# Performance work log

Measured on AMD Instinct MI355X. Metric: run time of the kernel, lower is better.

The kernel has to match this reference:

```python
import jax, jax.numpy as jnp
import numpy as np

D_MODEL = 1024
NUM_HEADS = 16
D_K = D_MODEL // NUM_HEADS  # 64
THETA = 10000.0


def apply_rope(x, positions, theta):
    # x: [b, h, s, d_k]; interleaved-pair RoPE
    d = x.shape[-1]
    inv_freq = theta ** (-jnp.arange(0, d, 2, dtype=jnp.float32) / d)  # [d/2]
    angles = positions.astype(jnp.float32)[:, None] * inv_freq[None, :]  # [s, d/2]
    cos = jnp.cos(angles)
    sin = jnp.sin(angles)
    x1 = x[..., 0::2]
    x2 = x[..., 1::2]
    out_even = x1 * cos - x2 * sin
    out_odd = x1 * sin + x2 * cos
    return jnp.stack([out_even, out_odd], axis=-1).reshape(x.shape)


def setup_inputs() -> dict:
    key = jax.random.key(0)
    kx, kq, kk, kv, ko = jax.random.split(key, 5)
    scale = 1.0 / np.sqrt(D_MODEL)
    return {
        "x": jax.random.normal(kx, (1, 4096, D_MODEL), dtype=jnp.float32),
        "Wq": jax.random.normal(kq, (D_MODEL, D_MODEL), dtype=jnp.float32) * scale,
        "Wk": jax.random.normal(kk, (D_MODEL, D_MODEL), dtype=jnp.float32) * scale,
        "Wv": jax.random.normal(kv, (D_MODEL, D_MODEL), dtype=jnp.float32) * scale,
        "Wo": jax.random.normal(ko, (D_MODEL, D_MODEL), dtype=jnp.float32) * scale,
    }


def reference(x, Wq, Wk, Wv, Wo):
    b, s, _ = x.shape
    # Linear (no bias, weight stored as [out, in]): y = x @ W^T
    q = jnp.einsum("bsd,ed->bse", x, Wq).reshape(b, s, NUM_HEADS, D_K).transpose(0, 2, 1, 3)
    k = jnp.einsum("bsd,ed->bse", x, Wk).reshape(b, s, NUM_HEADS, D_K).transpose(0, 2, 1, 3)
    v = jnp.einsum("bsd,ed->bse", x, Wv).reshape(b, s, NUM_HEADS, D_K).transpose(0, 2, 1, 3)

    positions = jnp.arange(s)
    q = apply_rope(q, positions, THETA)
    k = apply_rope(k, positions, THETA)

    scores = jnp.einsum("bhqd,bhkd->bhqk", q, k) / jnp.sqrt(jnp.float32(D_K))
    causal = jnp.tril(jnp.ones((s, s), dtype=bool))
    scores = jnp.where(causal, scores, -jnp.inf)
    probs = jax.nn.softmax(scores, axis=-1)
    ctx = jnp.einsum("bhqk,bhkd->bhqd", probs, v)  # [b,h,s,d_k]
    ctx = ctx.transpose(0, 2, 1, 3).reshape(b, s, D_MODEL)
    return jnp.einsum("bse,de->bsd", ctx, Wo)
```

## Files before the change

kernel.cpp:

```cpp
#include <hip/hip_runtime.h>
#include <hip/hip_bf16.h>
#include <math.h>


#define S_LEN 4096
#define DMODEL 1024
#define NHEAD 16
#define QSCALE 0.1803368801111244f
#define PSTR 76

typedef __attribute__((ext_vector_type(8))) short short8;
typedef __attribute__((ext_vector_type(4))) short short4_t;
typedef __attribute__((ext_vector_type(2))) unsigned int uint2_t;
typedef __attribute__((ext_vector_type(4))) float floatx4;

static __device__ __forceinline__ void load_lds16(const void* g, void* l) {
    __builtin_amdgcn_global_load_lds((const __attribute__((address_space(1))) void*)g,
                                     (__attribute__((address_space(3))) void*)l, 16, 0, 0);
}

static __device__ __forceinline__ __hip_bfloat16 bf16_fast(float f) {
    unsigned int u = __builtin_bit_cast(unsigned int, f) + 0x8000u;
    unsigned short s = (unsigned short)(u >> 16);
    return __builtin_bit_cast(__hip_bfloat16, s);
}
static __device__ __forceinline__ unsigned int pack_bf16x2(float a, float b) {
    unsigned int ua = __builtin_bit_cast(unsigned int, a) + 0x8000u;
    unsigned int ub = __builtin_bit_cast(unsigned int, b) + 0x8000u;
    return __builtin_amdgcn_perm(ub, ua, 0x07060302);
}

__global__ void cvt_all_kernel(const float* __restrict__ x,  const float* __restrict__ wq,
                               const float* __restrict__ wk, const float* __restrict__ wv,
                               const float* __restrict__ wo,
                               __hip_bfloat16* __restrict__ xb,  __hip_bfloat16* __restrict__ wqb,
                               __hip_bfloat16* __restrict__ wkb, __hip_bfloat16* __restrict__ wvb,
                               __hip_bfloat16* __restrict__ wob)
{
    const size_t NX = (size_t)S_LEN * DMODEL;
    const size_t NW = (size_t)DMODEL * DMODEL;
    size_t t = ((size_t)blockIdx.x * blockDim.x + threadIdx.x) * 4;
    const float* src; __hip_bfloat16* dst; size_t off;
    if (t < NX) { src = x; dst = xb; off = t; }
    else {
        size_t j = t - NX; int seg = (int)(j >> 20); off = j & (NW - 1);
        src = (seg == 0) ? wq : (seg == 1) ? wk : (seg == 2) ? wv : wo;
        dst = (seg == 0) ? wqb : (seg == 1) ? wkb : (seg == 2) ? wvb : wob;
    }
    float4 v = *(const float4*)(src + off);
    uint2_t w;
    w.x = pack_bf16x2(v.x, v.y);
    w.y = pack_bf16x2(v.z, v.w);
    *(uint2_t*)(dst + off) = w;
}

__global__ __launch_bounds__(256) void qkv_gemm(
    const __hip_bfloat16* __restrict__ A,
    const __hip_bfloat16* __restrict__ Bq,
    const __hip_bfloat16* __restrict__ Bk,
    const __hip_bfloat16* __restrict__ Bv,
    __hip_bfloat16* __restrict__ Qb,
    __hip_bfloat16* __restrict__ Kb,
    __hip_bfloat16* __restrict__ Vtb)
{
    __shared__ __hip_bfloat16 As[128 * 32];
    __shared__ __hip_bfloat16 Bs[128 * 32];
    const int tid  = threadIdx.x;
    const int wave = tid >> 6;
    const int lane = tid & 63;
    const int quad = lane >> 4;
    const int l15  = lane & 15;
    const int sec  = blockIdx.x >> 3;
    const __hip_bfloat16* B = (sec == 0) ? Bq : (sec == 1) ? Bk : Bv;
    const int n0 = (blockIdx.x & 7) * 128;
    const int m0 = blockIdx.y * 128;
    const int wm = (wave & 1) * 64;
    const int wn = (wave >> 1) * 64;

    floatx4 acc[4][4] = {};

    for (int kt = 0; kt < DMODEL; kt += 32) {
        #pragma unroll
        for (int p = 0; p < 2; ++p) {
            int base = (p * 4 + wave) * 1024;
            int b    = base + lane * 16;
            int row  = b >> 6;
            int ke   = (b & 63) >> 1;
            load_lds16(A + (size_t)(m0 + row) * DMODEL + kt + ke, (char*)As + base);
            load_lds16(B + (size_t)(n0 + row) * DMODEL + kt + ke, (char*)Bs + base);
        }
        __syncthreads();
        short8 af[4], bf[4];
        #pragma unroll
        for (int i = 0; i < 4; ++i)
            af[i] = *(const short8*)(As + (wm + i * 16 + l15) * 32 + quad * 8);
        #pragma unroll
        for (int j = 0; j < 4; ++j)
            bf[j] = *(const short8*)(Bs + (wn + j * 16 + l15) * 32 + quad * 8);
        #pragma unroll
        for (int i = 0; i < 4; ++i)
            #pragma unroll
            for (int j = 0; j < 4; ++j)
                acc[i][j] = __builtin_amdgcn_mfma_f32_16x16x32_bf16(af[i], bf[j], acc[i][j], 0, 0, 0);
        __syncthreads();
    }

    float ifreq[4];
    #pragma unroll
    for (int j = 0; j < 4; ++j) {
        int d = (j * 16 + l15) & 63;
        ifreq[j] = expf(-(float)(d & ~1) * (9.210340371976184f / 64.0f));
    }
    const float scale = (sec == 0) ? QSCALE : 1.0f;
    __hip_bfloat16* dst = (sec == 0) ? Qb : Kb;
    #pragma unroll
    for (int i = 0; i < 4; ++i) {
        int rowb = m0 + wm + i * 16 + quad * 4;
        #pragma unroll
        for (int j = 0; j < 4; ++j) {
            int col = n0 + wn + j * 16 + l15;
            int h   = col >> 6;
            int hd  = col & 63;
            if (sec == 2) {
                uint2_t w;
                w.x = pack_bf16x2(acc[i][j][0], acc[i][j][1]);
                w.y = pack_bf16x2(acc[i][j][2], acc[i][j][3]);
                int od = hd >> 4, lv = hd & 15;
                *(uint2_t*)(Vtb + (size_t)h * 262144 +
                            (((od * 512 + (rowb >> 3)) * 16 + lv) << 3) + (rowb & 7)) = w;
            } else {
                int g = hd >> 3, jj = hd & 7;
                #pragma unroll
                for (int r = 0; r < 4; ++r) {
                    int rr  = rowb + r;
                    float v = acc[i][j][r];
                    float ang = (float)rr * ifreq[j];
                    float sn, cs;
                    __sincosf(ang, &sn, &cs);
                    float pv  = __shfl_xor(v, 1);
                    float out = ((lane & 1) ? (pv * sn + v * cs)
                                            : (v * cs - pv * sn)) * scale;
                    dst[(size_t)h * 262144 +
                        ((((rr >> 4) * 8 + g) * 16 + (rr & 15)) << 3) + jj] = bf16_fast(out);
                }
            }
        }
    }
}

template<bool EDGE>
static __device__ __forceinline__ void attn_tile(
    int kt, int quad, int l15,
    const __hip_bfloat16* __restrict__ Kh, const __hip_bfloat16* __restrict__ Vh,
    const short8 aq[4][2], floatx4 o[4][4], float lp[4],
    __hip_bfloat16* __restrict__ PsW)
{
    asm volatile("s_waitcnt lgkmcnt(0)" ::: "memory");

    short8 kf[4][2], vf[4][2];
    #pragma unroll
    for (int ni = 0; ni < 4; ++ni)
        #pragma unroll
        for (int dc = 0; dc < 2; ++dc)
            kf[ni][dc] = *(const short8*)(Kh + (size_t)(((((kt*4 + ni)*8 + dc*4 + quad)*16 + l15) << 3)));
    #pragma unroll
    for (int od = 0; od < 4; ++od)
        #pragma unroll
        for (int dc = 0; dc < 2; ++dc)
            vf[od][dc] = *(const short8*)(Vh + (size_t)((((od*512 + kt*8 + dc*4 + quad)*16 + l15) << 3)));

    #pragma unroll
    for (int g = 0; g < 4; ++g) {
        __hip_bfloat16* strip = PsW + (g * 16 + l15) * PSTR;
        floatx4 st[4];
        #pragma unroll
        for (int ni = 0; ni < 4; ++ni) {
            floatx4 z = {};
            floatx4 s = __builtin_amdgcn_mfma_f32_16x16x32_bf16(kf[ni][0], aq[g][0], z, 0, 0, 0);
            st[ni]    = __builtin_amdgcn_mfma_f32_16x16x32_bf16(kf[ni][1], aq[g][1], s, 0, 0, 0);
        }
        #pragma unroll
        for (int ni = 0; ni < 4; ++ni) {
            float e[4];
            #pragma unroll
            for (int r = 0; r < 4; ++r) {
                float v = __builtin_amdgcn_exp2f(st[ni][r]);
                if (EDGE) {
                    if (ni * 16 + quad * 4 + r > g * 16 + l15) v = 0.0f;
                }
                e[r] = v;
            }
            lp[g] += (e[0] + e[1]) + (e[2] + e[3]);
            uint2_t w;
            w.x = pack_bf16x2(e[0], e[1]);
            w.y = pack_bf16x2(e[2], e[3]);
            *(short4_t*)(strip + ni * 16 + quad * 4) = __builtin_bit_cast(short4_t, w);
        }
        short8 ap[2];
        #pragma unroll
        for (int dc = 0; dc < 2; ++dc) {
            const __hip_bfloat16* pp = strip + dc * 32 + quad * 8;
            short4_t p0 = *(const short4_t*)pp;
            short4_t p1 = *(const short4_t*)(pp + 4);
            short8 a;
            a[0] = p0[0]; a[1] = p0[1]; a[2] = p0[2]; a[3] = p0[3];
            a[4] = p1[0]; a[5] = p1[1]; a[6] = p1[2]; a[7] = p1[3];
            ap[dc] = a;
        }
        #pragma unroll
        for (int od = 0; od < 4; ++od) {
            o[g][od] = __builtin_amdgcn_mfma_f32_16x16x32_bf16(ap[0], vf[od][0], o[g][od], 0, 0, 0);
            o[g][od] = __builtin_amdgcn_mfma_f32_16x16x32_bf16(ap[1], vf[od][1], o[g][od], 0, 0, 0);
        }
    }
}

__global__ __launch_bounds__(256, 2) void attn_kernel(
    const __hip_bfloat16* __restrict__ Q,
    const __hip_bfloat16* __restrict__ Kp,
    const __hip_bfloat16* __restrict__ Vp,
    __hip_bfloat16* __restrict__ CTX)
{
    __shared__ __hip_bfloat16 Buf[4][64 * PSTR];
    __shared__ float LPw[4][64];
    const int b  = blockIdx.x;
    const int h  = b & 15;
    const int u  = 63 - (b >> 4);
    const int tid  = threadIdx.x;
    const int wave = tid >> 6, lane = tid & 63;
    const int quad = lane >> 4, l15 = lane & 15;

    const __hip_bfloat16* Qh = Q  + (size_t)h * 262144;
    const __hip_bfloat16* Kh = Kp + (size_t)h * 262144;
    const __hip_bfloat16* Vh = Vp + (size_t)h * 262144;
    __hip_bfloat16* PsW = &Buf[wave][0];

    short8 aq[4][2];
    #pragma unroll
    for (int g = 0; g < 4; ++g)
        #pragma unroll
        for (int dc = 0; dc < 2; ++dc)
            aq[g][dc] = *(const short8*)(Qh + (size_t)(((((u*4 + g)*8 + dc*4 + quad)*16 + l15) << 3)));

    floatx4 o[4][4] = {};
    float lp[4] = {};

    for (int kt = wave; kt < u; kt += 4)
        attn_tile<false>(kt, quad, l15, Kh, Vh, aq, o, lp, PsW);
    if ((u & 3) == wave)
        attn_tile<true>(u, quad, l15, Kh, Vh, aq, o, lp, PsW);

    #pragma unroll
    for (int g = 0; g < 4; ++g) {
        float v = lp[g];
        v += __shfl_xor(v, 16);
        v += __shfl_xor(v, 32);
        lp[g] = v;
    }
    asm volatile("s_waitcnt lgkmcnt(0)" ::: "memory");
    if (quad == 0) {
        #pragma unroll
        for (int g = 0; g < 4; ++g)
            LPw[wave][g * 16 + l15] = lp[g];
    }
    #pragma unroll
    for (int g = 0; g < 4; ++g)
        #pragma unroll
        for (int od = 0; od < 4; ++od)
            #pragma unroll
            for (int r = 0; r < 4; ++r)
                Buf[wave][(g * 16 + quad * 4 + r) * PSTR + od * 16 + l15] =
                    bf16_fast(o[g][od][r]);
    __syncthreads();

    #pragma unroll
    for (int r = 0; r < 4; ++r) {
        int q = wave * 16 + quad * 4 + r;
        float ls = LPw[0][q] + LPw[1][q] + LPw[2][q] + LPw[3][q];
        float rl = __frcp_rn(ls);
        #pragma unroll
        for (int od = 0; od < 4; ++od) {
            float s = 0.0f;
            #pragma unroll
            for (int sl = 0; sl < 4; ++sl)
                s += __bfloat162float(Buf[sl][q * PSTR + od * 16 + l15]);
            CTX[(size_t)(u * 64 + q) * DMODEL + h * 64 + od * 16 + l15] =
                bf16_fast(s * rl);
        }
    }
}

__global__ __launch_bounds__(256) void out_gemm(
    const __hip_bfloat16* __restrict__ A,
    const __hip_bfloat16* __restrict__ B,
    float* __restrict__ C)
{
    __shared__ __hip_bfloat16 As[128 * 32];
    __shared__ __hip_bfloat16 Bs[64 * 32];
    const int tid  = threadIdx.x;
    const int wave = tid >> 6;
    const int lane = tid & 63;
    const int quad = lane >> 4;
    const int l15  = lane & 15;
    const int n0 = blockIdx.x * 64;
    const int m0 = blockIdx.y * 128;
    const int wm = (wave & 1) * 64;
    const int wn = (wave >> 1) * 32;

    floatx4 acc[4][2] = {};

    for (int kt = 0; kt < DMODEL; kt += 32) {
        #pragma unroll
        for (int p = 0; p < 3; ++p) {
            int id  = p * 4 + wave;
            if (id < 8) {
                int base = id * 1024;
                int b    = base + lane * 16;
                int row  = b >> 6;
                int ke   = (b & 63) >> 1;
                load_lds16(A + (size_t)(m0 + row) * DMODEL + kt + ke, (char*)As + base);
            } else {
                int base = (id - 8) * 1024;
                int b    = base + lane * 16;
                int row  = b >> 6;
                int ke   = (b & 63) >> 1;
                load_lds16(B + (size_t)(n0 + row) * DMODEL + kt + ke, (char*)Bs + base);
            }
        }
        __syncthreads();
        short8 af[4], bf[2];
        #pragma unroll
        for (int i = 0; i < 4; ++i)
            af[i] = *(const short8*)(As + (wm + i * 16 + l15) * 32 + quad * 8);
        #pragma unroll
        for (int j = 0; j < 2; ++j)
            bf[j] = *(const short8*)(Bs + (wn + j * 16 + l15) * 32 + quad * 8);
        #pragma unroll
        for (int i = 0; i < 4; ++i)
            #pragma unroll
            for (int j = 0; j < 2; ++j)
                acc[i][j] = __builtin_amdgcn_mfma_f32_16x16x32_bf16(af[i], bf[j], acc[i][j], 0, 0, 0);
        __syncthreads();
    }

    #pragma unroll
    for (int i = 0; i < 4; ++i) {
        int rowb = m0 + wm + i * 16 + quad * 4;
        #pragma unroll
        for (int j = 0; j < 2; ++j) {
            int col = n0 + wn + j * 16 + l15;
            #pragma unroll
            for (int r = 0; r < 4; ++r)
                C[(size_t)(rowb + r) * DMODEL + col] = acc[i][j][r];
        }
    }
}

extern "C" void kernel_launch(void* const* d_in, const int* in_sizes, int n_in,
                              void* d_out, int out_size, void* d_ws, size_t ws_size,
                              hipStream_t stream)
{
    const float* x  = (const float*)d_in[0];
    const float* Wq = (const float*)d_in[1];
    const float* Wk = (const float*)d_in[2];
    const float* Wv = (const float*)d_in[3];
    const float* Wo = (const float*)d_in[4];

    char* ws = (char*)d_ws;
    const size_t MB = 1024 * 1024;
    __hip_bfloat16* xb  = (__hip_bfloat16*)(ws);
    __hip_bfloat16* wqb = (__hip_bfloat16*)(ws +  8 * MB);
    __hip_bfloat16* wkb = (__hip_bfloat16*)(ws + 10 * MB);
    __hip_bfloat16* wvb = (__hip_bfloat16*)(ws + 12 * MB);
    __hip_bfloat16* wob = (__hip_bfloat16*)(ws + 14 * MB);
    __hip_bfloat16* Qb  = (__hip_bfloat16*)(ws + 16 * MB);
    __hip_bfloat16* Kbf = (__hip_bfloat16*)(ws + 24 * MB);
    __hip_bfloat16* Vtb = (__hip_bfloat16*)(ws + 32 * MB);
    __hip_bfloat16* Cx  = (__hip_bfloat16*)(ws + 40 * MB);

    cvt_all_kernel<<<8192, 256, 0, stream>>>(x, Wq, Wk, Wv, Wo, xb, wqb, wkb, wvb, wob);

    qkv_gemm<<<dim3(24, 32), 256, 0, stream>>>(xb, wqb, wkb, wvb, Qb, Kbf, Vtb);

    attn_kernel<<<1024, 256, 0, stream>>>(Qb, Kbf, Vtb, Cx);

    out_gemm<<<dim3(16, 32), 256, 0, stream>>>(Cx, wob, (float*)d_out);
}
```

Measured before the change: 202.4 us.

## Pre-swizzle bf16 operands in global memory and widen GEMM K-tile to 64

The conversion kernel and the attention epilogue now write the bf16 activations and weights with an XOR swizzle of 8-element groups inside each 64-wide K chunk. The GEMMs can then copy 64-wide K tiles straight into LDS with global_load_lds and read them without bank conflicts. Both QKV and output GEMMs double the K step to 64, halving the number of barrier pairs per tile at the cost of twice the LDS footprint. The conversion kernel also handles 8 elements per thread with half the blocks.

```diff
diff --git a/kernel.cpp b/kernel.cpp
--- a/kernel.cpp
+++ b/kernel.cpp
@@ -12,6 +12,7 @@
 typedef __attribute__((ext_vector_type(8))) short short8;
 typedef __attribute__((ext_vector_type(4))) short short4_t;
 typedef __attribute__((ext_vector_type(2))) unsigned int uint2_t;
+typedef __attribute__((ext_vector_type(4))) unsigned int uint4_t;
 typedef __attribute__((ext_vector_type(4))) float floatx4;
 
 static __device__ __forceinline__ void load_lds16(const void* g, void* l) {
@@ -39,7 +40,7 @@
 {
     const size_t NX = (size_t)S_LEN * DMODEL;
     const size_t NW = (size_t)DMODEL * DMODEL;
-    size_t t = ((size_t)blockIdx.x * blockDim.x + threadIdx.x) * 4;
+    size_t t = ((size_t)blockIdx.x * blockDim.x + threadIdx.x) * 8;
     const float* src; __hip_bfloat16* dst; size_t off;
     if (t < NX) { src = x; dst = xb; off = t; }
     else {
@@ -47,11 +48,18 @@
         src = (seg == 0) ? wq : (seg == 1) ? wk : (seg == 2) ? wv : wo;
         dst = (seg == 0) ? wqb : (seg == 1) ? wkb : (seg == 2) ? wvb : wob;
     }
-    float4 v = *(const float4*)(src + off);
-    uint2_t w;
-    w.x = pack_bf16x2(v.x, v.y);
-    w.y = pack_bf16x2(v.z, v.w);
-    *(uint2_t*)(dst + off) = w;
+    int row = (int)(off >> 10);
+    int k   = (int)(off & 1023);
+    int gp  = (((k >> 3) ^ row) & 7);
+    size_t doff = (off & ~(size_t)1023) + (size_t)((k & ~63) + (gp << 3));
+    float4 v0 = *(const float4*)(src + off);
+    float4 v1 = *(const float4*)(src + off + 4);
+    uint4_t w;
+    w.x = pack_bf16x2(v0.x, v0.y);
+    w.y = pack_bf16x2(v0.z, v0.w);
+    w.z = pack_bf16x2(v1.x, v1.y);
+    w.w = pack_bf16x2(v1.z, v1.w);
+    *(uint4_t*)(dst + doff) = w;
 }
 
 __global__ __launch_bounds__(256) void qkv_gemm(
@@ -63,13 +71,14 @@
     __hip_bfloat16* __restrict__ Kb,
     __hip_bfloat16* __restrict__ Vtb)
 {
-    __shared__ __hip_bfloat16 As[128 * 32];
-    __shared__ __hip_bfloat16 Bs[128 * 32];
+    __shared__ __hip_bfloat16 As[128 * 64];
+    __shared__ __hip_bfloat16 Bs[128 * 64];
     const int tid  = threadIdx.x;
     const int wave = tid >> 6;
     const int lane = tid & 63;
     const int quad = lane >> 4;
     const int l15  = lane & 15;
+    const int k7   = l15 & 7;
     const int sec  = blockIdx.x >> 3;
     const __hip_bfloat16* B = (sec == 0) ? Bq : (sec == 1) ? Bk : Bv;
     const int n0 = (blockIdx.x & 7) * 128;
@@ -79,29 +88,35 @@
 
     floatx4 acc[4][4] = {};
 
-    for (int kt = 0; kt < DMODEL; kt += 32) {
-        #pragma unroll
-        for (int p = 0; p < 2; ++p) {
-            int base = (p * 4 + wave) * 1024;
-            int b    = base + lane * 16;
-            int row  = b >> 6;
-            int ke   = (b & 63) >> 1;
-            load_lds16(A + (size_t)(m0 + row) * DMODEL + kt + ke, (char*)As + base);
-            load_lds16(B + (size_t)(n0 + row) * DMODEL + kt + ke, (char*)Bs + base);
+    for (int kt = 0; kt < DMODEL; kt += 64) {
+        #pragma unroll
+        for (int p = 0; p < 8; ++p) {
+            int id  = p * 4 + wave;
+            int cb  = (id & 15) * 1024;
+            int bb  = cb + lane * 16;
+            int row = bb >> 7;
+            int ce  = (bb & 127) >> 1;
+            if (id < 16)
+                load_lds16(A + (size_t)(m0 + row) * DMODEL + kt + ce, (char*)As + cb);
+            else
+                load_lds16(B + (size_t)(n0 + row) * DMODEL + kt + ce, (char*)Bs + cb);
         }
         __syncthreads();
-        short8 af[4], bf[4];
-        #pragma unroll
-        for (int i = 0; i < 4; ++i)
-            af[i] = *(const short8*)(As + (wm + i * 16 + l15) * 32 + quad * 8);
-        #pragma unroll
-        for (int j = 0; j < 4; ++j)
-            bf[j] = *(const short8*)(Bs + (wn + j * 16 + l15) * 32 + quad * 8);
-        #pragma unroll
-        for (int i = 0; i < 4; ++i)
+        #pragma unroll
+        for (int dc = 0; dc < 2; ++dc) {
+            short8 af[4], bf[4];
+            #pragma unroll
+            for (int i = 0; i < 4; ++i)
+                af[i] = *(const short8*)(As + (wm + i * 16 + l15) * 64 + (((dc * 4 + quad) ^ k7) << 3));
             #pragma unroll
             for (int j = 0; j < 4; ++j)
-                acc[i][j] = __builtin_amdgcn_mfma_f32_16x16x32_bf16(af[i], bf[j], acc[i][j], 0, 0, 0);
+                bf[j] = *(const short8*)(Bs + (wn + j * 16 + l15) * 64 + (((dc * 4 + quad) ^ k7) << 3));
+            #pragma unroll
+            for (int i = 0; i < 4; ++i)
+                #pragma unroll
+                for (int j = 0; j < 4; ++j)
+                    acc[i][j] = __builtin_amdgcn_mfma_f32_16x16x32_bf16(af[i], bf[j], acc[i][j], 0, 0, 0);
+        }
         __syncthreads();
     }
 
@@ -275,7 +290,8 @@
 
     #pragma unroll
     for (int r = 0; r < 4; ++r) {
-        int q = wave * 16 + quad * 4 + r;
+        int q   = wave * 16 + quad * 4 + r;
+        int row = u * 64 + q;
         float ls = LPw[0][q] + LPw[1][q] + LPw[2][q] + LPw[3][q];
         float rl = __frcp_rn(ls);
         #pragma unroll
@@ -284,7 +300,9 @@
             #pragma unroll
             for (int sl = 0; sl < 4; ++sl)
                 s += __bfloat162float(Buf[sl][q * PSTR + od * 16 + l15]);
-            CTX[(size_t)(u * 64 + q) * DMODEL + h * 64 + od * 16 + l15] =
+            int cidx = od * 16 + l15;
+            int gp   = (((cidx >> 3) ^ row) & 7);
+            CTX[(size_t)row * DMODEL + h * 64 + (gp << 3) + (cidx & 7)] =
                 bf16_fast(s * rl);
         }
     }
@@ -295,13 +313,14 @@
     const __hip_bfloat16* __restrict__ B,
     float* __restrict__ C)
 {
-    __shared__ __hip_bfloat16 As[128 * 32];
-    __shared__ __hip_bfloat16 Bs[64 * 32];
+    __shared__ __hip_bfloat16 As[128 * 64];
+    __shared__ __hip_bfloat16 Bs[64 * 64];
     const int tid  = threadIdx.x;
     const int wave = tid >> 6;
     const int lane = tid & 63;
     const int quad = lane >> 4;
     const int l15  = lane & 15;
+    const int k7   = l15 & 7;
     const int n0 = blockIdx.x * 64;
     const int m0 = blockIdx.y * 128;
     const int wm = (wave & 1) * 64;
@@ -309,37 +328,40 @@
 
     floatx4 acc[4][2] = {};
 
-    for (int kt = 0; kt < DMODEL; kt += 32) {
-        #pragma unroll
-        for (int p = 0; p < 3; ++p) {
+    for (int kt = 0; kt < DMODEL; kt += 64) {
+        #pragma unroll
+        for (int p = 0; p < 6; ++p) {
             int id  = p * 4 + wave;
-            if (id < 8) {
-                int base = id * 1024;
-                int b    = base + lane * 16;
-                int row  = b >> 6;
-                int ke   = (b & 63) >> 1;
-                load_lds16(A + (size_t)(m0 + row) * DMODEL + kt + ke, (char*)As + base);
+            if (id < 16) {
+                int cb  = id * 1024;
+                int bb  = cb + lane * 16;
+                int row = bb >> 7;
+                int ce  = (bb & 127) >> 1;
+                load_lds16(A + (size_t)(m0 + row) * DMODEL + kt + ce, (char*)As + cb);
             } else {
-                int base = (id - 8) * 1024;
-                int b    = base + lane * 16;
-                int row  = b >> 6;
-                int ke   = (b & 63) >> 1;
-                load_lds16(B + (size_t)(n0 + row) * DMODEL + kt + ke, (char*)Bs + base);
+                int cb  = (id - 16) * 1024;
+                int bb  = cb + lane * 16;
+                int row = bb >> 7;
+                int ce  = (bb & 127) >> 1;
+                load_lds16(B + (size_t)(n0 + row) * DMODEL + kt + ce, (char*)Bs + cb);
             }
         }
         __syncthreads();
-        short8 af[4], bf[2];
-        #pragma unroll
-        for (int i = 0; i < 4; ++i)
-            af[i] = *(const short8*)(As + (wm + i * 16 + l15) * 32 + quad * 8);
-        #pragma unroll
-        for (int j = 0; j < 2; ++j)
-            bf[j] = *(const short8*)(Bs + (wn + j * 16 + l15) * 32 + quad * 8);
-        #pragma unroll
-        for (int i = 0; i < 4; ++i)
+        #pragma unroll
+        for (int dc = 0; dc < 2; ++dc) {
+            short8 af[4], bf[2];
+            #pragma unroll
+            for (int i = 0; i < 4; ++i)
+                af[i] = *(const short8*)(As + (wm + i * 16 + l15) * 64 + (((dc * 4 + quad) ^ k7) << 3));
             #pragma unroll
             for (int j = 0; j < 2; ++j)
-                acc[i][j] = __builtin_amdgcn_mfma_f32_16x16x32_bf16(af[i], bf[j], acc[i][j], 0, 0, 0);
+                bf[j] = *(const short8*)(Bs + (wn + j * 16 + l15) * 64 + (((dc * 4 + quad) ^ k7) << 3));
+            #pragma unroll
+            for (int i = 0; i < 4; ++i)
+                #pragma unroll
+                for (int j = 0; j < 2; ++j)
+                    acc[i][j] = __builtin_amdgcn_mfma_f32_16x16x32_bf16(af[i], bf[j], acc[i][j], 0, 0, 0);
+        }
         __syncthreads();
     }
 
@@ -378,7 +400,7 @@
     __hip_bfloat16* Vtb = (__hip_bfloat16*)(ws + 32 * MB);
     __hip_bfloat16* Cx  = (__hip_bfloat16*)(ws + 40 * MB);
 
-    cvt_all_kernel<<<8192, 256, 0, stream>>>(x, Wq, Wk, Wv, Wo, xb, wqb, wkb, wvb, wob);
+    cvt_all_kernel<<<4096, 256, 0, stream>>>(x, Wq, Wk, Wv, Wo, xb, wqb, wkb, wvb, wob);
 
     qkv_gemm<<<dim3(24, 32), 256, 0, stream>>>(xb, wqb, wkb, wvb, Qb, Kbf, Vtb);
 
```

Result: faster. 189.3 us (-6.5%).
